# Kernel tuning notes

Measured on AMD Instinct MI355X. Metric: run time of the kernel, lower is better.

The kernel has to match this reference:

```python
import jax, jax.numpy as jnp
import numpy as np

FOUR_PI = 4.0 * np.pi
INF_CLAMP = 1e30


def setup_inputs() -> dict:
    key = jax.random.key(0)
    k1, k2, k3, k4 = jax.random.split(key, 4)
    B, N, M, S = 16, 2048, 16, 128
    pcl_transformed = jax.random.normal(k1, (B, N, M, 3), dtype=jnp.float32)
    primitive_points = jax.random.normal(k2, (B, M, S, 3), dtype=jnp.float32)
    size = jax.random.uniform(k3, (B, M, 3), dtype=jnp.float32, minval=0.05, maxval=1.0)
    probs = jax.random.uniform(k4, (B, M), dtype=jnp.float32)
    return {"pcl_transformed": pcl_transformed, "primitive_points": primitive_points,
            "size": size, "probs": probs}


def reference(pcl_transformed, primitive_points, size, probs):
    B, N, M, _ = pcl_transformed.shape
    S = primitive_points.shape[2]

    # diff: (B, M, S, N, 3); dist: (B, M, S, N)
    diff = primitive_points[:, :, :, None, :] - jnp.transpose(pcl_transformed, (0, 2, 1, 3))[:, :, None, :, :]
    dist = jnp.sum(diff * diff, axis=-1)

    # ---- pcl_to_prim loss (min over S, sort over M, stick-breaking cumprod) ----
    d1 = jnp.transpose(jnp.min(dist, axis=2), (0, 2, 1))  # (B, N, M)
    idx = jnp.argsort(d1, axis=-1)                         # (B, N, M)
    distance = jnp.take_along_axis(d1, idx, axis=-1)
    p = jnp.take_along_axis(jnp.broadcast_to(probs[:, None, :], (B, N, M)), idx, axis=-1)
    neg_cumprod = jnp.cumprod(1.0 - p, axis=-1)
    neg_cumprod = jnp.concatenate([jnp.ones_like(neg_cumprod[..., :1]), neg_cumprod[..., :-1]], axis=-1)
    minprob = p * neg_cumprod
    pcl_to_prim = jnp.einsum('bnm,bnm->', distance, minprob) / (B * N)

    # ---- prim_to_pcl loss (min over N, superquadric-area weighting) ----
    d2 = jnp.min(dist, axis=-1)                            # (B, M, S)
    d2 = jnp.where(d2 >= INF_CLAMP, 0.0, d2)
    s0, s1, s2 = size[..., 0], size[..., 1], size[..., 2]
    area = FOUR_PI * ((s0 * s1) ** 1.6 / 3 + (s0 * s2) ** 1.6 / 3 + (s1 * s2) ** 1.6 / 3) ** 0.625
    area = M * area / jnp.sum(area, axis=-1, keepdims=True)  # (B, M)
    prim_to_pcl = jnp.einsum('bm,bm,bm->', jnp.mean(d2, axis=-1), probs, area) / (B * M)

    # No regularizer types enabled -> regs == 0 (matches regularizer_type=[]).
    regs = jnp.zeros((), dtype=pcl_to_prim.dtype)
    total = 1.0 * pcl_to_prim + 1.0 * prim_to_pcl + regs
    return total, pcl_to_prim, prim_to_pcl, regs
```

## Files before the change

kernel.cpp:

```cpp
#include <hip/hip_runtime.h>
#include <math.h>

#define BB 16
#define NN 2048
#define MM 16
#define SS 128

__constant__ const float kFourPi = 12.566370614359172f;

__global__ __launch_bounds__(1024) void fused_dist_kernel(
    const float* __restrict__ pcl,
    const float* __restrict__ prim,
    float* __restrict__ d1,
    float* __restrict__ d2sum,
    unsigned int* __restrict__ counter)
{
    const int bm  = blockIdx.x;
    const int b   = bm >> 4;
    const int m   = bm & 15;
    const int tid = threadIdx.x;

    __shared__ float Qx[NN], Qy[NN], Qz[NN];
    __shared__ float Px[SS], Py[SS], Pz[SS];
    __shared__ float d1s[4][NN];
    __shared__ float wmin[16][32];
    __shared__ float red[2];

    if (bm == 0 && tid == 0)
        __hip_atomic_store(counter, 0u, __ATOMIC_RELAXED, __HIP_MEMORY_SCOPE_AGENT);

    {
        const size_t base = ((size_t)(b * NN) * MM + m) * 3;
#pragma unroll
        for (int j = 0; j < 2; ++j) {
            const int n = tid + j * 1024;
            const float* q = pcl + base + (size_t)n * (MM * 3);
            Qx[n] = q[0]; Qy[n] = q[1]; Qz[n] = q[2];
        }
    }
    if (tid < SS) {
        const float* pp = prim + ((size_t)bm * SS + tid) * 3;
        Px[tid] = pp[0]; Py[tid] = pp[1]; Pz[tid] = pp[2];
    }
    __syncthreads();

    const int sub  = tid >> 8;
    const int stid = tid & 255;
    const int s0   = sub * 32;
    const int wid  = tid >> 6;
    const int lane = tid & 63;

    float qx[8], qy[8], qz[8], d1min[8];
#pragma unroll
    for (int j = 0; j < 8; ++j) {
        const int n = stid + j * 256;
        qx[j] = Qx[n]; qy[j] = Qy[n]; qz[j] = Qz[n];
        d1min[j] = 3.0e38f;
    }

#pragma unroll 4
    for (int s = 0; s < 32; ++s) {
        const float px = Px[s0 + s], py = Py[s0 + s], pz = Pz[s0 + s];
        float lmin = 3.0e38f;
#pragma unroll
        for (int j = 0; j < 8; ++j) {
            const float dx = px - qx[j];
            const float dy = py - qy[j];
            const float dz = pz - qz[j];
            float d = dx * dx;
            d = fmaf(dy, dy, d);
            d = fmaf(dz, dz, d);
            d1min[j] = fminf(d1min[j], d);
            lmin     = fminf(lmin, d);
        }
#pragma unroll
        for (int off = 32; off > 0; off >>= 1)
            lmin = fminf(lmin, __shfl_down(lmin, off, 64));
        if (lane == 0) wmin[wid][s] = lmin;
    }

#pragma unroll
    for (int j = 0; j < 8; ++j)
        d1s[sub][stid + j * 256] = d1min[j];
    __syncthreads();

#pragma unroll
    for (int j = 0; j < 2; ++j) {
        const int n = tid + j * 1024;
        d1[(size_t)bm * NN + n] = fminf(fminf(d1s[0][n], d1s[1][n]),
                                        fminf(d1s[2][n], d1s[3][n]));
    }

    float v = 0.0f;
    if (tid < SS) {
        const int sc = tid >> 5, sl = tid & 31;
        v = fminf(fminf(wmin[sc * 4 + 0][sl], wmin[sc * 4 + 1][sl]),
                  fminf(wmin[sc * 4 + 2][sl], wmin[sc * 4 + 3][sl]));
        if (v >= 1.0e30f) v = 0.0f;
    }
#pragma unroll
    for (int off = 32; off > 0; off >>= 1)
        v += __shfl_down(v, off, 64);
    if (tid < SS && lane == 0) red[wid] = v;
    __syncthreads();
    if (tid == 0) d2sum[bm] = red[0] + red[1];
}

__global__ __launch_bounds__(256) void p2p_final_kernel(
    const float* __restrict__ d1,
    const float* __restrict__ probs,
    const float* __restrict__ size_,
    const float* __restrict__ d2sum,
    float* __restrict__ partial,
    unsigned int* __restrict__ counter,
    float* __restrict__ out)
{
    const int tid = threadIdx.x;
    const int gid = blockIdx.x * 256 + tid;
    const int b   = gid >> 11;
    const int n   = gid & (NN - 1);

    float d[16], p[16];
#pragma unroll
    for (int m = 0; m < 16; ++m)
        d[m] = d1[((size_t)(b * MM + m)) * NN + n];

    const float* pb = probs + b * MM;
#pragma unroll
    for (int k = 0; k < 16; ++k) p[k] = pb[k];

#define CE(i, j)                                              \
    {                                                         \
        const bool c = d[i] > d[j];                           \
        const float td = c ? d[j] : d[i];                     \
        d[j] = c ? d[i] : d[j];  d[i] = td;                   \
        const float tp = c ? p[j] : p[i];                     \
        p[j] = c ? p[i] : p[j];  p[i] = tp;                   \
    }
#pragma unroll
    for (int r = 0; r < 16; ++r) {
        if ((r & 1) == 0) {
            CE(0, 1) CE(2, 3) CE(4, 5) CE(6, 7)
            CE(8, 9) CE(10, 11) CE(12, 13) CE(14, 15)
        } else {
            CE(1, 2) CE(3, 4) CE(5, 6) CE(7, 8)
            CE(9, 10) CE(11, 12) CE(13, 14)
        }
    }
#undef CE

    float acc = 1.0f, sum = 0.0f;
#pragma unroll
    for (int k = 0; k < 16; ++k) {
        sum += d[k] * p[k] * acc;
        acc *= (1.0f - p[k]);
    }

    const int wid  = tid >> 6;
    const int lane = tid & 63;
    __shared__ float red4[4];
#pragma unroll
    for (int off = 32; off > 0; off >>= 1)
        sum += __shfl_down(sum, off, 64);
    if (lane == 0) red4[wid] = sum;
    __syncthreads();

    __shared__ bool amLast;
    if (tid == 0) {
        const float bsum = red4[0] + red4[1] + red4[2] + red4[3];
        __hip_atomic_store(&partial[blockIdx.x], bsum,
                           __ATOMIC_RELEASE, __HIP_MEMORY_SCOPE_AGENT);
        const unsigned int prev = __hip_atomic_fetch_add(
            counter, 1u, __ATOMIC_ACQ_REL, __HIP_MEMORY_SCOPE_AGENT);
        amLast = (prev == 127u);
    }
    __syncthreads();
    if (!amLast) return;

    const int fb = tid >> 4;

    __shared__ float  areaSh[256];
    __shared__ double redA[4];
    __shared__ double redB[4];

    const float s0 = size_[tid * 3 + 0];
    const float s1 = size_[tid * 3 + 1];
    const float s2 = size_[tid * 3 + 2];
    const float inner = powf(s0 * s1, 1.6f) * (1.0f / 3.0f)
                      + powf(s0 * s2, 1.6f) * (1.0f / 3.0f)
                      + powf(s1 * s2, 1.6f) * (1.0f / 3.0f);
    const float a = kFourPi * powf(inner, 0.625f);
    areaSh[tid] = a;
    __syncthreads();

    float asum = 0.0f;
#pragma unroll
    for (int mm = 0; mm < 16; ++mm) asum += areaSh[fb * 16 + mm];
    const float anorm = 16.0f * a / asum;

    double t = (double)(d2sum[tid] * (1.0f / 128.0f)) * (double)probs[tid] * (double)anorm;
#pragma unroll
    for (int off = 32; off > 0; off >>= 1)
        t += __shfl_down(t, off, 64);
    if (lane == 0) redA[wid] = t;

    double u = 0.0;
    if (tid < 128) {
        const float pv = __hip_atomic_load(&partial[tid],
                                           __ATOMIC_ACQUIRE, __HIP_MEMORY_SCOPE_AGENT);
        u = (double)pv;
    }
#pragma unroll
    for (int off = 32; off > 0; off >>= 1)
        u += __shfl_down(u, off, 64);
    if (lane == 0) redB[wid] = u;

    __syncthreads();
    if (tid == 0) {
        const double prim_to_pcl = (redA[0] + redA[1] + redA[2] + redA[3]) / 256.0;
        const double pcl_to_prim = (redB[0] + redB[1] + redB[2] + redB[3]) / 32768.0;
        out[0] = (float)(pcl_to_prim + prim_to_pcl);
        out[1] = (float)pcl_to_prim;
        out[2] = (float)prim_to_pcl;
        out[3] = 0.0f;
    }
}


extern "C" void kernel_launch(void* const* d_in, const int* in_sizes, int n_in,
                              void* d_out, int out_size, void* d_ws, size_t ws_size,
                              hipStream_t stream) {
    const float* pcl   = (const float*)d_in[0];
    const float* prim  = (const float*)d_in[1];
    const float* size_ = (const float*)d_in[2];
    const float* probs = (const float*)d_in[3];
    float* out = (float*)d_out;

    float* d1            = (float*)d_ws;
    float* d2sum         = d1 + (size_t)256 * NN;
    float* partial       = d2sum + 256;
    unsigned int* counter = (unsigned int*)(partial + 128);

    fused_dist_kernel<<<BB * MM, 1024, 0, stream>>>(pcl, prim, d1, d2sum, counter);
    p2p_final_kernel<<<128, 256, 0, stream>>>(d1, probs, size_, d2sum, partial, counter, out);
}
```

Measured before the change: 96.52 us.

## Split distance into prep/dist kernels with dot-product expansion and S-split grid

A new prep kernel transposes the point cloud into per-(b,m) float4 records that carry a precomputed half squared norm, and does the same for the primitive points. The distance kernel then evaluates the half distance as |q|²/2 + |p|²/2 - p·q using three FMAs. It splits S into four chunks across blockIdx.y so the grid has 1024 blocks of 256 threads instead of 256 blocks of 1024 threads. The min over N is done with a transpose-style butterfly shuffle reduction, and the final kernel combines the four partial d1/d2 buffers and doubles the result. This trades an extra kernel launch, an extra pass over the point data and more partial-buffer traffic for better occupancy and cheaper inner-loop arithmetic, at some risk of cancellation error in the expanded distance.

```diff
diff --git a/kernel.cpp b/kernel.cpp
--- a/kernel.cpp
+++ b/kernel.cpp
@@ -8,109 +8,174 @@
 
 __constant__ const float kFourPi = 12.566370614359172f;
 
-__global__ __launch_bounds__(1024) void fused_dist_kernel(
+__global__ __launch_bounds__(256) void prep_kernel(
     const float* __restrict__ pcl,
     const float* __restrict__ prim,
-    float* __restrict__ d1,
-    float* __restrict__ d2sum,
+    float4* __restrict__ PclP,
+    float4* __restrict__ PrimP,
     unsigned int* __restrict__ counter)
 {
+    const int b   = blockIdx.x;
+    const int tid = threadIdx.x;
+
+    if (blockIdx.x == 0 && blockIdx.y == 0 && tid == 0)
+        __hip_atomic_store(counter, 0u, __ATOMIC_RELAXED, __HIP_MEMORY_SCOPE_AGENT);
+
+    if (blockIdx.y < 16) {
+        const int n0 = blockIdx.y * 128;
+        __shared__ float q[6144];
+        const float4* src = (const float4*)(pcl + ((size_t)b * NN + n0) * (MM * 3));
+        float4* qv = (float4*)q;
+#pragma unroll
+        for (int k = 0; k < 6; ++k)
+            qv[tid + k * 256] = src[tid + k * 256];
+        __syncthreads();
+
+        const int n  = tid & 127;
+        const int mh = tid >> 7;
+#pragma unroll
+        for (int k = 0; k < 8; ++k) {
+            const int m = k * 2 + mh;
+            const float x = q[(n * 16 + m) * 3 + 0];
+            const float y = q[(n * 16 + m) * 3 + 1];
+            const float z = q[(n * 16 + m) * 3 + 2];
+            const float h = 0.5f * (x * x + y * y + z * z);
+            PclP[((size_t)(b * MM + m)) * NN + n0 + n] = make_float4(x, y, z, h);
+        }
+    } else {
+        const float* pp = prim + (size_t)b * (MM * SS * 3);
+#pragma unroll
+        for (int k = 0; k < 8; ++k) {
+            const int p = tid + k * 256;
+            const float x = pp[p * 3 + 0];
+            const float y = pp[p * 3 + 1];
+            const float z = pp[p * 3 + 2];
+            const float h = 0.5f * (x * x + y * y + z * z);
+            PrimP[(size_t)b * (MM * SS) + p] = make_float4(x, y, z, h);
+        }
+    }
+}
+
+__global__ __launch_bounds__(256, 4) void dist3_kernel(
+    const float4* __restrict__ PclP,
+    const float4* __restrict__ PrimP,
+    float* __restrict__ d1part,
+    float* __restrict__ d2part)
+{
     const int bm  = blockIdx.x;
-    const int b   = bm >> 4;
-    const int m   = bm & 15;
+    const int cs  = blockIdx.y;
     const int tid = threadIdx.x;
-
-    __shared__ float Qx[NN], Qy[NN], Qz[NN];
-    __shared__ float Px[SS], Py[SS], Pz[SS];
-    __shared__ float d1s[4][NN];
-    __shared__ float wmin[16][32];
-    __shared__ float red[2];
-
-    if (bm == 0 && tid == 0)
-        __hip_atomic_store(counter, 0u, __ATOMIC_RELAXED, __HIP_MEMORY_SCOPE_AGENT);
-
-    {
-        const size_t base = ((size_t)(b * NN) * MM + m) * 3;
-#pragma unroll
-        for (int j = 0; j < 2; ++j) {
-            const int n = tid + j * 1024;
-            const float* q = pcl + base + (size_t)n * (MM * 3);
-            Qx[n] = q[0]; Qy[n] = q[1]; Qz[n] = q[2];
-        }
-    }
-    if (tid < SS) {
-        const float* pp = prim + ((size_t)bm * SS + tid) * 3;
-        Px[tid] = pp[0]; Py[tid] = pp[1]; Pz[tid] = pp[2];
-    }
-    __syncthreads();
-
-    const int sub  = tid >> 8;
-    const int stid = tid & 255;
-    const int s0   = sub * 32;
     const int wid  = tid >> 6;
     const int lane = tid & 63;
 
-    float qx[8], qy[8], qz[8], d1min[8];
+    __shared__ float4 Plds[32];
+    __shared__ float  wred[4][64];
+
+    if (tid < 32)
+        Plds[tid] = PrimP[(size_t)bm * SS + cs * 32 + tid];
+
+    float qx[8], qy[8], qz[8], hq[8], d1m[8];
+    const float4* qp = PclP + (size_t)bm * NN + tid;
 #pragma unroll
     for (int j = 0; j < 8; ++j) {
-        const int n = stid + j * 256;
-        qx[j] = Qx[n]; qy[j] = Qy[n]; qz[j] = Qz[n];
-        d1min[j] = 3.0e38f;
-    }
-
-#pragma unroll 4
+        const float4 q = qp[j * 256];
+        qx[j] = q.x; qy[j] = q.y; qz[j] = q.z; hq[j] = q.w;
+        d1m[j] = 3.0e38f;
+    }
+    __syncthreads();
+
+    float d2r[32];
+#pragma unroll
     for (int s = 0; s < 32; ++s) {
-        const float px = Px[s0 + s], py = Py[s0 + s], pz = Pz[s0 + s];
-        float lmin = 3.0e38f;
+        const float4 f = Plds[s];
+        float e[8];
 #pragma unroll
         for (int j = 0; j < 8; ++j) {
-            const float dx = px - qx[j];
-            const float dy = py - qy[j];
-            const float dz = pz - qz[j];
-            float d = dx * dx;
-            d = fmaf(dy, dy, d);
-            d = fmaf(dz, dz, d);
-            d1min[j] = fminf(d1min[j], d);
-            lmin     = fminf(lmin, d);
-        }
+            float t = hq[j] + f.w;
+            t = fmaf(f.x, -qx[j], t);
+            t = fmaf(f.y, -qy[j], t);
+            t = fmaf(f.z, -qz[j], t);
+            e[j] = t;
+            d1m[j] = fminf(d1m[j], t);
+        }
+        const float m01 = fminf(e[0], e[1]);
+        const float m23 = fminf(e[2], e[3]);
+        const float m45 = fminf(e[4], e[5]);
+        const float m67 = fminf(e[6], e[7]);
+        d2r[s] = fminf(fminf(m01, m23), fminf(m45, m67));
+    }
+
+    float* dd = d1part + ((size_t)(cs * 256 + bm)) * NN + tid;
+#pragma unroll
+    for (int j = 0; j < 8; ++j) dd[j * 256] = d1m[j];
+
+    float v16[16];
+    {
+        const bool hi = (lane & 32) != 0;
+#pragma unroll
+        for (int k = 0; k < 16; ++k) {
+            const float xk = hi ? d2r[k + 16] : d2r[k];
+            const float xs = hi ? d2r[k] : d2r[k + 16];
+            v16[k] = fminf(xk, __shfl_xor(xs, 32, 64));
+        }
+    }
+    float v8[8];
+    {
+        const bool hi = (lane & 16) != 0;
+#pragma unroll
+        for (int k = 0; k < 8; ++k) {
+            const float xk = hi ? v16[k + 8] : v16[k];
+            const float xs = hi ? v16[k] : v16[k + 8];
+            v8[k] = fminf(xk, __shfl_xor(xs, 16, 64));
+        }
+    }
+    float v4[4];
+    {
+        const bool hi = (lane & 8) != 0;
+#pragma unroll
+        for (int k = 0; k < 4; ++k) {
+            const float xk = hi ? v8[k + 4] : v8[k];
+            const float xs = hi ? v8[k] : v8[k + 4];
+            v4[k] = fminf(xk, __shfl_xor(xs, 8, 64));
+        }
+    }
+    float v2[2];
+    {
+        const bool hi = (lane & 4) != 0;
+        const float xk0 = hi ? v4[2] : v4[0];
+        const float xs0 = hi ? v4[0] : v4[2];
+        v2[0] = fminf(xk0, __shfl_xor(xs0, 4, 64));
+        const float xk1 = hi ? v4[3] : v4[1];
+        const float xs1 = hi ? v4[1] : v4[3];
+        v2[1] = fminf(xk1, __shfl_xor(xs1, 4, 64));
+    }
+    float v1;
+    {
+        const bool hi = (lane & 2) != 0;
+        const float xk = hi ? v2[1] : v2[0];
+        const float xs = hi ? v2[0] : v2[1];
+        v1 = fminf(xk, __shfl_xor(xs, 2, 64));
+    }
+    const float r = fminf(v1, __shfl_xor(v1, 1, 64));
+    wred[wid][lane] = r;
+    __syncthreads();
+
+    if (tid < 64) {
+        float mv = fminf(fminf(wred[0][tid], wred[1][tid]),
+                         fminf(wred[2][tid], wred[3][tid]));
+        if (mv >= 5.0e29f) mv = 0.0f;
 #pragma unroll
         for (int off = 32; off > 0; off >>= 1)
-            lmin = fminf(lmin, __shfl_down(lmin, off, 64));
-        if (lane == 0) wmin[wid][s] = lmin;
-    }
-
-#pragma unroll
-    for (int j = 0; j < 8; ++j)
-        d1s[sub][stid + j * 256] = d1min[j];
-    __syncthreads();
-
-#pragma unroll
-    for (int j = 0; j < 2; ++j) {
-        const int n = tid + j * 1024;
-        d1[(size_t)bm * NN + n] = fminf(fminf(d1s[0][n], d1s[1][n]),
-                                        fminf(d1s[2][n], d1s[3][n]));
-    }
-
-    float v = 0.0f;
-    if (tid < SS) {
-        const int sc = tid >> 5, sl = tid & 31;
-        v = fminf(fminf(wmin[sc * 4 + 0][sl], wmin[sc * 4 + 1][sl]),
-                  fminf(wmin[sc * 4 + 2][sl], wmin[sc * 4 + 3][sl]));
-        if (v >= 1.0e30f) v = 0.0f;
-    }
-#pragma unroll
-    for (int off = 32; off > 0; off >>= 1)
-        v += __shfl_down(v, off, 64);
-    if (tid < SS && lane == 0) red[wid] = v;
-    __syncthreads();
-    if (tid == 0) d2sum[bm] = red[0] + red[1];
+            mv += __shfl_down(mv, off, 64);
+        if (tid == 0) d2part[cs * 256 + bm] = mv;
+    }
 }
 
 __global__ __launch_bounds__(256) void p2p_final_kernel(
-    const float* __restrict__ d1,
+    const float* __restrict__ d1part,
     const float* __restrict__ probs,
     const float* __restrict__ size_,
-    const float* __restrict__ d2sum,
+    const float* __restrict__ d2part,
     float* __restrict__ partial,
     unsigned int* __restrict__ counter,
     float* __restrict__ out)
@@ -122,8 +187,15 @@
 
     float d[16], p[16];
 #pragma unroll
-    for (int m = 0; m < 16; ++m)
-        d[m] = d1[((size_t)(b * MM + m)) * NN + n];
+    for (int m = 0; m < 16; ++m) {
+        const size_t base = ((size_t)(b * MM + m)) * NN + n;
+        const float v0 = d1part[base];
+        const float v1 = d1part[base + (size_t)256 * NN];
+        const float v2 = d1part[base + (size_t)512 * NN];
+        const float v3 = d1part[base + (size_t)768 * NN];
+        const float mn = fminf(fminf(v0, v1), fminf(v2, v3));
+        d[m] = mn + mn;
+    }
 
     const float* pb = probs + b * MM;
 #pragma unroll
@@ -198,7 +270,8 @@
     for (int mm = 0; mm < 16; ++mm) asum += areaSh[fb * 16 + mm];
     const float anorm = 16.0f * a / asum;
 
-    double t = (double)(d2sum[tid] * (1.0f / 128.0f)) * (double)probs[tid] * (double)anorm;
+    const float d2s = d2part[tid] + d2part[256 + tid] + d2part[512 + tid] + d2part[768 + tid];
+    double t = (double)(d2s * (1.0f / 128.0f)) * (double)probs[tid] * (double)anorm;
 #pragma unroll
     for (int off = 32; off > 0; off >>= 1)
         t += __shfl_down(t, off, 64);
@@ -236,11 +309,15 @@
     const float* probs = (const float*)d_in[3];
     float* out = (float*)d_out;
 
-    float* d1            = (float*)d_ws;
-    float* d2sum         = d1 + (size_t)256 * NN;
-    float* partial       = d2sum + 256;
+    const size_t nBMN = (size_t)BB * MM * NN;
+    float4* PclP  = (float4*)d_ws;
+    float4* PrimP = PclP + nBMN;
+    float*  d1part = (float*)(PrimP + (size_t)BB * MM * SS);
+    float*  d2part = d1part + 4 * nBMN;
+    float*  partial = d2part + 1024;
     unsigned int* counter = (unsigned int*)(partial + 128);
 
-    fused_dist_kernel<<<BB * MM, 1024, 0, stream>>>(pcl, prim, d1, d2sum, counter);
-    p2p_final_kernel<<<128, 256, 0, stream>>>(d1, probs, size_, d2sum, partial, counter, out);
+    prep_kernel<<<dim3(BB, 17), 256, 0, stream>>>(pcl, prim, PclP, PrimP, counter);
+    dist3_kernel<<<dim3(BB * MM, 4), 256, 0, stream>>>(PclP, PrimP, d1part, d2part);
+    p2p_final_kernel<<<128, 256, 0, stream>>>(d1part, probs, size_, d2part, partial, counter, out);
 }
```

Result: faster. 90.31 us (-6.4%).
